# Kernel tuning notes

Measured on AMD Instinct MI355X. Metric: run time of the kernel, lower is better.

The kernel has to match this reference:

```python
import jax, jax.numpy as jnp
import numpy as np

N_NODES = 50000
N_EDGES = 600000
N_PAIRS = 200000
D_IN, D_HID = 128, 256


def _sage_conv(x, src, dst, W_l, b_l, W_r, num_nodes):
    # PyG SAGEConv('mean'): out = mean_agg(x_j) @ W_l + b_l + x @ W_r
    msgs = x[src]                                              # [E, d] gather
    agg = jax.ops.segment_sum(msgs, dst, num_segments=num_nodes)
    deg = jax.ops.segment_sum(jnp.ones((src.shape[0],), x.dtype), dst,
                              num_segments=num_nodes)
    agg = agg / jnp.maximum(deg, 1.0)[:, None]                 # mean, safe for deg=0
    return agg @ W_l + b_l + x @ W_r


def setup_inputs() -> dict:
    key = jax.random.key(0)
    ks = jax.random.split(key, 8)
    s = lambda d: 1.0 / np.sqrt(d)
    return {
        "features": jax.random.normal(ks[0], (N_NODES, D_IN), jnp.float32),
        "edge_index": jax.random.randint(ks[1], (2, N_EDGES), 0, N_NODES, jnp.int64),
        "mask": jax.random.randint(ks[2], (N_PAIRS, 2), 0, N_NODES, jnp.int64),
        "W1l": jax.random.normal(ks[3], (D_IN, D_HID), jnp.float32) * s(D_IN),
        "b1l": jnp.zeros((D_HID,), jnp.float32),
        "W1r": jax.random.normal(ks[4], (D_IN, D_HID), jnp.float32) * s(D_IN),
        "W2l": jax.random.normal(ks[5], (D_HID, D_IN), jnp.float32) * s(D_HID),
        "b2l": jnp.zeros((D_IN,), jnp.float32),
        "W2r": jax.random.normal(ks[6], (D_HID, D_IN), jnp.float32) * s(D_HID),
        "Wlin": jax.random.normal(ks[7], (2 * D_IN, 1), jnp.float32) * s(2 * D_IN),
        "blin": jnp.zeros((1,), jnp.float32),
    }


def reference(features, edge_index, mask, W1l, b1l, W1r, W2l, b2l, W2r, Wlin, blin):
    n = features.shape[0]
    src, dst = edge_index[0], edge_index[1]
    h = _sage_conv(features, src, dst, W1l, b1l, W1r, n)       # [N, 256]
    h = jax.nn.relu(h)                                         # dropout p=0 -> identity
    h = _sage_conv(h, src, dst, W2l, b2l, W2r, n)              # [N, 128]
    m = mask.T                                                 # [2, P]
    p1 = jax.lax.stop_gradient(h[m[0]])                        # detach in original
    p2 = jax.lax.stop_gradient(h[m[1]])
    pair = jnp.concatenate((p1, p2), axis=1)                   # [P, 256]
    return jax.nn.sigmoid(pair @ Wlin + blin)                  # [P, 1]
```

## Files before the change

### kernel.cpp

```cpp
#include <hip/hip_runtime.h>
#include <math.h>

#define NN 50000
#define NE 600000
#define NP 200000
#define NB_SCAN 49

typedef unsigned int uint;
typedef unsigned short ushort;
typedef __attribute__((ext_vector_type(8))) short bf16x8;
typedef __attribute__((ext_vector_type(4))) float f32x4;

__device__ __forceinline__ ushort f2bf(float f) {
    uint u = __float_as_uint(f);
    uint r = (u + 0x7FFFu + ((u >> 16) & 1u)) >> 16;
    return (ushort)r;
}
__device__ __forceinline__ float bf2f(uint lo16) {
    return __uint_as_float(lo16 << 16);
}

__device__ __forceinline__ int wave_iscan(int v, int lane) {
#pragma unroll
    for (int off = 1; off < 64; off <<= 1) {
        int t = __shfl_up(v, off, 64);
        if (lane >= off) v += t;
    }
    return v;
}

typedef const __attribute__((address_space(1))) uint* gas_ptr;
typedef __attribute__((address_space(3))) uint* las_ptr;
__device__ __forceinline__ void gload_lds16(const uint* g, uint* l) {
    __builtin_amdgcn_global_load_lds((gas_ptr)(void*)g, (las_ptr)(void*)l, 16, 0, 0);
}

__device__ __forceinline__ void acc8(float* a, uint4 v) {
    a[0] += bf2f(v.x & 0xffffu); a[1] += bf2f(v.x >> 16);
    a[2] += bf2f(v.y & 0xffffu); a[3] += bf2f(v.y >> 16);
    a[4] += bf2f(v.z & 0xffffu); a[5] += bf2f(v.z >> 16);
    a[6] += bf2f(v.w & 0xffffu); a[7] += bf2f(v.w >> 16);
}

template <int K, int N>
__device__ __forceinline__ void prepB_one(int idx, const float* __restrict__ Wt,
                                          const float* __restrict__ Wb,
                                          ushort* __restrict__ Bp) {
    int lane = idx & 63;
    int nt = (idx >> 6) % (N / 16);
    int ct = idx / (64 * (N / 16));
    int n = nt * 16 + (lane & 15);
    int kb = ct * 32 + (lane >> 4) * 8;
#pragma unroll
    for (int j = 0; j < 8; j++) {
        int k = kb + j;
        float w = (k < K / 2) ? Wt[(size_t)k * N + n] : Wb[(size_t)(k - K / 2) * N + n];
        Bp[(size_t)idx * 8 + j] = f2bf(w);
    }
}

#define T_PREP (NN * 32)
#define T_DEG  (T_PREP + NE)
#define T_B1   (T_DEG + 8192)
#define T_PQ   (T_B1 + 1024)
#define T_CAB  (T_PQ + 2)
__global__ void k_pre(const float* __restrict__ x, uint* __restrict__ xb,
                      const int* __restrict__ dst, int* __restrict__ deg,
                      const float* __restrict__ W1l, const float* __restrict__ W1r,
                      ushort* __restrict__ Bp1,
                      const float* __restrict__ W2l, const float* __restrict__ W2r,
                      const float* __restrict__ Wlin, const float* __restrict__ b2l,
                      float* __restrict__ pq, float* __restrict__ cab) {
    int t = blockIdx.x * 256 + threadIdx.x;
    if (t < T_PREP) {
        int n = t >> 5, c4 = t & 31;
        float4 v = *(const float4*)(x + (size_t)n * 128 + c4 * 4);
        uint2 o;
        o.x = (uint)f2bf(v.x) | ((uint)f2bf(v.y) << 16);
        o.y = (uint)f2bf(v.z) | ((uint)f2bf(v.w) << 16);
        *(uint2*)(xb + (size_t)n * 64 + c4 * 2) = o;
    } else if (t < T_DEG) {
        atomicAdd(deg + dst[t - T_PREP], 1);
    } else if (t < T_B1) {
        prepB_one<256, 256>(t - T_DEG, W1l, W1r, Bp1);
    } else if (t < T_PQ) {
        int idx = t - T_B1;
        int vec = idx >> 8;
        int k = idx & 255;
        const float* W = (vec < 2) ? W2l : W2r;
        const float* wl = Wlin + (vec & 1) * 128;
        float s = 0.f;
#pragma unroll 4
        for (int j = 0; j < 128; j++) s += W[(size_t)k * 128 + j] * wl[j];
        pq[idx] = s;
    } else if (t < T_CAB) {
        int i = t - T_PQ;
        float s = 0.f;
        for (int j = 0; j < 128; j++) s += b2l[j] * Wlin[i * 128 + j];
        cab[i] = s;
    }
}

__global__ __launch_bounds__(1024) void k_scan(const int* __restrict__ deg,
                                               int* __restrict__ bsum,
                                               int* __restrict__ flags,
                                               int* __restrict__ rowptr,
                                               int* __restrict__ cursor) {
    int tid = threadIdx.x;
    int i = blockIdx.x * 1024 + tid;
    int lane = tid & 63, wid = tid >> 6;
    int v = (i < NN) ? deg[i] : 0;
    int incl = wave_iscan(v, lane);
    __shared__ int wt[16];
    __shared__ int sboff;
    if (lane == 63) wt[wid] = incl;
    __syncthreads();
    if (tid < 16) {
        int w = wt[tid];
#pragma unroll
        for (int off = 1; off < 16; off <<= 1) {
            int t = __shfl_up(w, off, 64);
            if (tid >= off) w += t;
        }
        wt[tid] = w;
    }
    __syncthreads();
    int base = (wid > 0) ? wt[wid - 1] : 0;
    int excl_local = incl - v + base;
    if (tid == 0)
        __hip_atomic_store(&bsum[blockIdx.x], wt[15], __ATOMIC_RELEASE,
                           __HIP_MEMORY_SCOPE_AGENT);
    __syncthreads();
    if (tid == 0) {
        __hip_atomic_fetch_add(&flags[0], 1, __ATOMIC_ACQ_REL, __HIP_MEMORY_SCOPE_AGENT);
        while (__hip_atomic_load(&flags[0], __ATOMIC_ACQUIRE,
                                 __HIP_MEMORY_SCOPE_AGENT) < NB_SCAN) {}
    }
    __syncthreads();
    if (tid < 64) {
        int b = (tid < NB_SCAN && tid < (int)blockIdx.x)
                    ? __hip_atomic_load(&bsum[tid], __ATOMIC_ACQUIRE,
                                        __HIP_MEMORY_SCOPE_AGENT)
                    : 0;
#pragma unroll
        for (int off = 1; off < 64; off <<= 1) b += __shfl_xor(b, off, 64);
        if (tid == 0) sboff = b;
    }
    __syncthreads();
    int boff = sboff;
    if (i < NN) {
        int rv = excl_local + boff;
        rowptr[i] = rv;
        cursor[i] = rv;
    }
    if (i == 0) rowptr[NN] = NE;
}

__global__ void k_fill(const int* __restrict__ src, const int* __restrict__ dst,
                       int* __restrict__ cursor, int* __restrict__ ssrc) {
    int e0 = (blockIdx.x * 256 + threadIdx.x) * 4;
    if (e0 >= NE) return;
    int4 d4 = *(const int4*)(dst + e0);
    int4 s4 = *(const int4*)(src + e0);
    int p0 = atomicAdd(cursor + d4.x, 1);
    int p1 = atomicAdd(cursor + d4.y, 1);
    int p2 = atomicAdd(cursor + d4.z, 1);
    int p3 = atomicAdd(cursor + d4.w, 1);
    ssrc[p0] = s4.x;
    ssrc[p1] = s4.y;
    ssrc[p2] = s4.z;
    ssrc[p3] = s4.w;
}

__global__ void k_agg1(const uint* __restrict__ xb, uint* __restrict__ aggb,
                       const int* __restrict__ rowptr, const int* __restrict__ ssrc) {
    int t = blockIdx.x * 256 + threadIdx.x;
    int n = t >> 6;
    if (n >= NN) return;
    int lane = t & 63;
    int g = lane >> 4;
    int s = lane & 15;
    int r0 = rowptr[n], r1 = rowptr[n + 1];
    float a0[8] = {0.f, 0.f, 0.f, 0.f, 0.f, 0.f, 0.f, 0.f};
    float a1[8] = {0.f, 0.f, 0.f, 0.f, 0.f, 0.f, 0.f, 0.f};
    int e = r0;
    for (; e + 16 <= r1; e += 16) {
        int i0 = ssrc[e + g];
        int i1 = ssrc[e + 4 + g];
        int i2 = ssrc[e + 8 + g];
        int i3 = ssrc[e + 12 + g];
        uint4 v0 = *(const uint4*)(xb + (size_t)i0 * 64 + s * 4);
        uint4 v1 = *(const uint4*)(xb + (size_t)i1 * 64 + s * 4);
        uint4 v2 = *(const uint4*)(xb + (size_t)i2 * 64 + s * 4);
        uint4 v3 = *(const uint4*)(xb + (size_t)i3 * 64 + s * 4);
        acc8(a0, v0); acc8(a1, v1); acc8(a0, v2); acc8(a1, v3);
    }
    if (e + 8 <= r1) {
        int i0 = ssrc[e + g];
        int i1 = ssrc[e + 4 + g];
        uint4 v0 = *(const uint4*)(xb + (size_t)i0 * 64 + s * 4);
        uint4 v1 = *(const uint4*)(xb + (size_t)i1 * 64 + s * 4);
        acc8(a0, v0); acc8(a1, v1);
        e += 8;
    }
    if (e + 4 <= r1) {
        int i0 = ssrc[e + g];
        uint4 v0 = *(const uint4*)(xb + (size_t)i0 * 64 + s * 4);
        acc8(a0, v0);
        e += 4;
    }
    int rem = r1 - e;
    if (g < rem) {
        int i0 = ssrc[e + g];
        uint4 v0 = *(const uint4*)(xb + (size_t)i0 * 64 + s * 4);
        acc8(a1, v0);
    }
    float ax[8];
#pragma unroll
    for (int j = 0; j < 8; j++) ax[j] = a0[j] + a1[j];
#pragma unroll
    for (int j = 0; j < 8; j++) {
        ax[j] += __shfl_xor(ax[j], 16, 64);
        ax[j] += __shfl_xor(ax[j], 32, 64);
    }
    if (g == 0) {
        float sc = 1.0f / fmaxf((float)(r1 - r0), 1.0f);
        uint4 o;
        o.x = (uint)f2bf(ax[0] * sc) | ((uint)f2bf(ax[1] * sc) << 16);
        o.y = (uint)f2bf(ax[2] * sc) | ((uint)f2bf(ax[3] * sc) << 16);
        o.z = (uint)f2bf(ax[4] * sc) | ((uint)f2bf(ax[5] * sc) << 16);
        o.w = (uint)f2bf(ax[6] * sc) | ((uint)f2bf(ax[7] * sc) << 16);
        *(uint4*)(aggb + (size_t)n * 64 + s * 4) = o;
    }
}

__global__ __launch_bounds__(256) void k_gemm1(const uint* __restrict__ agg,
                                               const uint* __restrict__ xbu,
                                               const ushort* __restrict__ Bp,
                                               const float* __restrict__ bias,
                                               const float* __restrict__ pq,
                                               float2* __restrict__ g2,
                                               float2* __restrict__ u2) {
    __shared__ uint Af[16 * 256];
    __shared__ float red[4][4][32];
    const int NTW = 4;
    int wave = threadIdx.x >> 6;
    int lane = threadIdx.x & 63;
    int quad = lane >> 4;
    int l15 = lane & 15;
    int mbase = blockIdx.x * 32;

#pragma unroll
    for (int i = 0; i < 4; i++) {
        int chunk = wave * 4 + i;
        int rt = chunk >> 3;
        int ct = chunk & 7;
        int node = mbase + rt * 16 + l15;
        if (node >= NN) node = NN - 1;
        const uint* srcp = ((ct < 4) ? agg : xbu)
                           + (size_t)node * 64 + (ct & 3) * 16 + quad * 4;
        gload_lds16(srcp, &Af[chunk * 256 + lane * 4]);
    }
    __syncthreads();

    f32x4 acc0[NTW], acc1[NTW];
#pragma unroll
    for (int i = 0; i < NTW; i++) {
        acc0[i] = (f32x4){0.f, 0.f, 0.f, 0.f};
        acc1[i] = (f32x4){0.f, 0.f, 0.f, 0.f};
    }
    const bf16x8* bp = (const bf16x8*)Bp;
#pragma unroll
    for (int ct = 0; ct < 8; ct++) {
        bf16x8 a0 = *(const bf16x8*)(&Af[ct * 256 + lane * 4]);
        bf16x8 a1 = *(const bf16x8*)(&Af[(8 + ct) * 256 + lane * 4]);
#pragma unroll
        for (int ntl = 0; ntl < NTW; ntl++) {
            int nt = wave * NTW + ntl;
            bf16x8 b = bp[(ct * 16 + nt) * 64 + lane];
            acc0[ntl] = __builtin_amdgcn_mfma_f32_16x16x32_bf16(a0, b, acc0[ntl], 0, 0, 0);
            acc1[ntl] = __builtin_amdgcn_mfma_f32_16x16x32_bf16(a1, b, acc1[ntl], 0, 0, 0);
        }
    }
    float pga[2][4] = {{0,0,0,0},{0,0,0,0}}, pgb[2][4] = {{0,0,0,0},{0,0,0,0}};
    float pua[2][4] = {{0,0,0,0},{0,0,0,0}}, pub[2][4] = {{0,0,0,0},{0,0,0,0}};
#pragma unroll
    for (int ntl = 0; ntl < NTW; ntl++) {
        int col = (wave * NTW + ntl) * 16 + l15;
        float bv = bias[col];
        float wpa = pq[col], wpb = pq[256 + col];
        float wqa = pq[512 + col], wqb = pq[768 + col];
#pragma unroll
        for (int reg = 0; reg < 4; reg++) {
            float v0 = acc0[ntl][reg] + bv;  v0 = v0 > 0.f ? v0 : 0.f;
            float v1 = acc1[ntl][reg] + bv;  v1 = v1 > 0.f ? v1 : 0.f;
            pga[0][reg] += v0 * wpa;  pgb[0][reg] += v0 * wpb;
            pua[0][reg] += v0 * wqa;  pub[0][reg] += v0 * wqb;
            pga[1][reg] += v1 * wpa;  pgb[1][reg] += v1 * wpb;
            pua[1][reg] += v1 * wqa;  pub[1][reg] += v1 * wqb;
        }
    }
#pragma unroll
    for (int off = 1; off < 16; off <<= 1) {
#pragma unroll
        for (int rt = 0; rt < 2; rt++) {
#pragma unroll
            for (int reg = 0; reg < 4; reg++) {
                pga[rt][reg] += __shfl_xor(pga[rt][reg], off, 64);
                pgb[rt][reg] += __shfl_xor(pgb[rt][reg], off, 64);
                pua[rt][reg] += __shfl_xor(pua[rt][reg], off, 64);
                pub[rt][reg] += __shfl_xor(pub[rt][reg], off, 64);
            }
        }
    }
    if (l15 == 0) {
#pragma unroll
        for (int rt = 0; rt < 2; rt++) {
#pragma unroll
            for (int reg = 0; reg < 4; reg++) {
                int row = rt * 16 + quad * 4 + reg;
                red[0][wave][row] = pga[rt][reg];
                red[1][wave][row] = pgb[rt][reg];
                red[2][wave][row] = pua[rt][reg];
                red[3][wave][row] = pub[rt][reg];
            }
        }
    }
    __syncthreads();
    if (threadIdx.x < 32) {
        int row = threadIdx.x;
        int m = mbase + row;
        if (m < NN) {
            float ga = (red[0][0][row] + red[0][1][row]) + (red[0][2][row] + red[0][3][row]);
            float gb = (red[1][0][row] + red[1][1][row]) + (red[1][2][row] + red[1][3][row]);
            float ua = (red[2][0][row] + red[2][1][row]) + (red[2][2][row] + red[2][3][row]);
            float ub = (red[3][0][row] + red[3][1][row]) + (red[3][2][row] + red[3][3][row]);
            g2[m] = make_float2(ga, gb);
            u2[m] = make_float2(ua, ub);
        }
    }
}

__global__ void k_sagg(const float2* __restrict__ g2, const float2* __restrict__ u2,
                       const int* __restrict__ rowptr, const int* __restrict__ ssrc,
                       const float* __restrict__ cab,
                       float* __restrict__ sa, float* __restrict__ sb) {
    int n = blockIdx.x * 256 + threadIdx.x;
    if (n >= NN) return;
    int r0 = rowptr[n], r1 = rowptr[n + 1];
    float a0 = 0.f, b0 = 0.f, a1 = 0.f, b1 = 0.f;
    float a2 = 0.f, b2 = 0.f, a3 = 0.f, b3 = 0.f;
    int e = r0;
    for (; e + 4 <= r1; e += 4) {
        float2 v0 = g2[ssrc[e]];
        float2 v1 = g2[ssrc[e + 1]];
        float2 v2 = g2[ssrc[e + 2]];
        float2 v3 = g2[ssrc[e + 3]];
        a0 += v0.x; b0 += v0.y;
        a1 += v1.x; b1 += v1.y;
        a2 += v2.x; b2 += v2.y;
        a3 += v3.x; b3 += v3.y;
    }
    for (; e < r1; e++) {
        float2 v = g2[ssrc[e]];
        a0 += v.x; b0 += v.y;
    }
    float sc = 1.0f / fmaxf((float)(r1 - r0), 1.0f);
    float2 u = u2[n];
    sa[n] = ((a0 + a1) + (a2 + a3)) * sc + u.x + cab[0];
    sb[n] = ((b0 + b1) + (b2 + b3)) * sc + u.y + cab[1];
}

__global__ void k_pairs(const float* __restrict__ sa, const float* __restrict__ sb,
                        const int* __restrict__ mask, const float* __restrict__ blin,
                        float* __restrict__ out) {
    int p = blockIdx.x * 256 + threadIdx.x;
    if (p >= NP) return;
    int2 m = ((const int2*)mask)[p];
    float v = sa[m.x] + sb[m.y] + blin[0];
    out[p] = 1.0f / (1.0f + __expf(-v));
}

extern "C" void kernel_launch(void* const* d_in, const int* in_sizes, int n_in,
                              void* d_out, int out_size, void* d_ws, size_t ws_size,
                              hipStream_t stream) {
    const float* x    = (const float*)d_in[0];
    const int*   ei   = (const int*)  d_in[1];
    const int*   mask = (const int*)  d_in[2];
    const float* W1l  = (const float*)d_in[3];
    const float* b1l  = (const float*)d_in[4];
    const float* W1r  = (const float*)d_in[5];
    const float* W2l  = (const float*)d_in[6];
    const float* b2l  = (const float*)d_in[7];
    const float* W2r  = (const float*)d_in[8];
    const float* Wlin = (const float*)d_in[9];
    const float* blin = (const float*)d_in[10];
    float* out = (float*)d_out;

    const int* src = ei;
    const int* dst = ei + NE;

    char* ws = (char*)d_ws;
    int*    deg    = (int*)(ws);
    int*    flags  = (int*)(ws + 0xF0000);
    int*    rowptr = (int*)(ws + (size_t)1 * (1 << 20));
    int*    cursor = (int*)(ws + (size_t)2 * (1 << 20));
    int*    ssrc   = (int*)(ws + (size_t)3 * (1 << 20));
    int*    bsum   = (int*)(ws + (size_t)6 * (1 << 20));
    ushort* Bp1    = (ushort*)(ws + (size_t)8 * (1 << 20));
    float*  pq     = (float*)(ws + (size_t)9 * (1 << 20));
    float*  cab    = (float*)(ws + (size_t)9 * (1 << 20) + 65536);
    float*  sa     = (float*)(ws + (size_t)10 * (1 << 20));
    float*  sb     = (float*)(ws + (size_t)11 * (1 << 20));
    float2* g2     = (float2*)(ws + (size_t)12 * (1 << 20));
    float2* u2     = (float2*)(ws + (size_t)13 * (1 << 20));
    uint*   xb     = (uint*)(ws + (size_t)14 * (1 << 20));
    uint*   aggb   = (uint*)(ws + (size_t)28 * (1 << 20));

    hipMemsetAsync(ws, 0, (size_t)1 << 20, stream);

    k_pre  <<<(T_CAB + 255) / 256, 256, 0, stream>>>(x, xb, dst, deg,
                                                     W1l, W1r, Bp1,
                                                     W2l, W2r, Wlin, b2l, pq, cab);
    k_scan <<<NB_SCAN, 1024, 0, stream>>>(deg, bsum, flags, rowptr, cursor);
    k_fill <<<(NE / 4 + 255) / 256, 256, 0, stream>>>(src, dst, cursor, ssrc);
    k_agg1 <<<NN / 4, 256, 0, stream>>>(xb, aggb, rowptr, ssrc);
    k_gemm1<<<(NN + 31) / 32, 256, 0, stream>>>(aggb, xb, Bp1, b1l, pq, g2, u2);
    k_sagg <<<(NN + 255) / 256, 256, 0, stream>>>(g2, u2, rowptr, ssrc, cab, sa, sb);
    k_pairs<<<(NP + 255) / 256, 256, 0, stream>>>(sa, sb, mask, blin, out);
}
```

Baseline: 216.6 us.

## Partition CSR fill by destination range and double rows per GEMM block

The CSR fill kernel now splits edges into chunks and launches 8 partitions per chunk. Each block reads its chunk of edges but only scatters edges whose destination falls in its node range, which keeps atomic and scatter traffic local to a smaller region of memory (intended for L2 locality). The cost is reading src/dst 8 times. Separately, the first-layer GEMM processes 64 rows per block instead of 32, so each B-fragment load feeds twice as many MFMAs, at the cost of more registers and LDS and fewer blocks.

```diff
diff --git a/kernel.cpp b/kernel.cpp
--- a/kernel.cpp
+++ b/kernel.cpp
@@ -5,6 +5,10 @@
 #define NE 600000
 #define NP 200000
 #define NB_SCAN 49
+#define NPART 8
+#define PART_N (NN / NPART)
+#define FILL_CHUNKS 75
+#define CHUNK_E (NE / FILL_CHUNKS)
 
 typedef unsigned int uint;
 typedef unsigned short ushort;
@@ -158,18 +162,19 @@
 
 __global__ void k_fill(const int* __restrict__ src, const int* __restrict__ dst,
                        int* __restrict__ cursor, int* __restrict__ ssrc) {
-    int e0 = (blockIdx.x * 256 + threadIdx.x) * 4;
-    if (e0 >= NE) return;
-    int4 d4 = *(const int4*)(dst + e0);
-    int4 s4 = *(const int4*)(src + e0);
-    int p0 = atomicAdd(cursor + d4.x, 1);
-    int p1 = atomicAdd(cursor + d4.y, 1);
-    int p2 = atomicAdd(cursor + d4.z, 1);
-    int p3 = atomicAdd(cursor + d4.w, 1);
-    ssrc[p0] = s4.x;
-    ssrc[p1] = s4.y;
-    ssrc[p2] = s4.z;
-    ssrc[p3] = s4.w;
+    int part = blockIdx.x & 7;
+    int chunk = blockIdx.x >> 3;
+    int lo = part * PART_N;
+    int e_begin = chunk * CHUNK_E;
+    int e_end = e_begin + CHUNK_E;
+    for (int e0 = e_begin + threadIdx.x * 4; e0 < e_end; e0 += 1024) {
+        int4 d4 = *(const int4*)(dst + e0);
+        int4 s4 = *(const int4*)(src + e0);
+        if ((uint)(d4.x - lo) < (uint)PART_N) ssrc[atomicAdd(cursor + d4.x, 1)] = s4.x;
+        if ((uint)(d4.y - lo) < (uint)PART_N) ssrc[atomicAdd(cursor + d4.y, 1)] = s4.y;
+        if ((uint)(d4.z - lo) < (uint)PART_N) ssrc[atomicAdd(cursor + d4.z, 1)] = s4.z;
+        if ((uint)(d4.w - lo) < (uint)PART_N) ssrc[atomicAdd(cursor + d4.w, 1)] = s4.w;
+    }
 }
 
 __global__ void k_agg1(const uint* __restrict__ xb, uint* __restrict__ aggb,
@@ -241,18 +246,18 @@
                                                const float* __restrict__ pq,
                                                float2* __restrict__ g2,
                                                float2* __restrict__ u2) {
-    __shared__ uint Af[16 * 256];
-    __shared__ float red[4][4][32];
+    __shared__ uint Af[32 * 256];
+    __shared__ float red[4][4][64];
     const int NTW = 4;
     int wave = threadIdx.x >> 6;
     int lane = threadIdx.x & 63;
     int quad = lane >> 4;
     int l15 = lane & 15;
-    int mbase = blockIdx.x * 32;
-
-#pragma unroll
-    for (int i = 0; i < 4; i++) {
-        int chunk = wave * 4 + i;
+    int mbase = blockIdx.x * 64;
+
+#pragma unroll
+    for (int i = 0; i < 8; i++) {
+        int chunk = wave * 8 + i;
         int rt = chunk >> 3;
         int ct = chunk & 7;
         int node = mbase + rt * 16 + l15;
@@ -263,27 +268,36 @@
     }
     __syncthreads();
 
-    f32x4 acc0[NTW], acc1[NTW];
-#pragma unroll
-    for (int i = 0; i < NTW; i++) {
-        acc0[i] = (f32x4){0.f, 0.f, 0.f, 0.f};
-        acc1[i] = (f32x4){0.f, 0.f, 0.f, 0.f};
-    }
+    f32x4 acc[4][NTW];
+#pragma unroll
+    for (int rt = 0; rt < 4; rt++)
+#pragma unroll
+        for (int i = 0; i < NTW; i++) acc[rt][i] = (f32x4){0.f, 0.f, 0.f, 0.f};
     const bf16x8* bp = (const bf16x8*)Bp;
 #pragma unroll
     for (int ct = 0; ct < 8; ct++) {
-        bf16x8 a0 = *(const bf16x8*)(&Af[ct * 256 + lane * 4]);
-        bf16x8 a1 = *(const bf16x8*)(&Af[(8 + ct) * 256 + lane * 4]);
+        bf16x8 a0 = *(const bf16x8*)(&Af[(0 * 8 + ct) * 256 + lane * 4]);
+        bf16x8 a1 = *(const bf16x8*)(&Af[(1 * 8 + ct) * 256 + lane * 4]);
+        bf16x8 a2 = *(const bf16x8*)(&Af[(2 * 8 + ct) * 256 + lane * 4]);
+        bf16x8 a3 = *(const bf16x8*)(&Af[(3 * 8 + ct) * 256 + lane * 4]);
 #pragma unroll
         for (int ntl = 0; ntl < NTW; ntl++) {
             int nt = wave * NTW + ntl;
             bf16x8 b = bp[(ct * 16 + nt) * 64 + lane];
-            acc0[ntl] = __builtin_amdgcn_mfma_f32_16x16x32_bf16(a0, b, acc0[ntl], 0, 0, 0);
-            acc1[ntl] = __builtin_amdgcn_mfma_f32_16x16x32_bf16(a1, b, acc1[ntl], 0, 0, 0);
-        }
-    }
-    float pga[2][4] = {{0,0,0,0},{0,0,0,0}}, pgb[2][4] = {{0,0,0,0},{0,0,0,0}};
-    float pua[2][4] = {{0,0,0,0},{0,0,0,0}}, pub[2][4] = {{0,0,0,0},{0,0,0,0}};
+            acc[0][ntl] = __builtin_amdgcn_mfma_f32_16x16x32_bf16(a0, b, acc[0][ntl], 0, 0, 0);
+            acc[1][ntl] = __builtin_amdgcn_mfma_f32_16x16x32_bf16(a1, b, acc[1][ntl], 0, 0, 0);
+            acc[2][ntl] = __builtin_amdgcn_mfma_f32_16x16x32_bf16(a2, b, acc[2][ntl], 0, 0, 0);
+            acc[3][ntl] = __builtin_amdgcn_mfma_f32_16x16x32_bf16(a3, b, acc[3][ntl], 0, 0, 0);
+        }
+    }
+    float pga[4][4], pgb[4][4], pua[4][4], pub[4][4];
+#pragma unroll
+    for (int rt = 0; rt < 4; rt++)
+#pragma unroll
+        for (int reg = 0; reg < 4; reg++) {
+            pga[rt][reg] = 0.f; pgb[rt][reg] = 0.f;
+            pua[rt][reg] = 0.f; pub[rt][reg] = 0.f;
+        }
 #pragma unroll
     for (int ntl = 0; ntl < NTW; ntl++) {
         int col = (wave * NTW + ntl) * 16 + l15;
@@ -291,19 +305,20 @@
         float wpa = pq[col], wpb = pq[256 + col];
         float wqa = pq[512 + col], wqb = pq[768 + col];
 #pragma unroll
-        for (int reg = 0; reg < 4; reg++) {
-            float v0 = acc0[ntl][reg] + bv;  v0 = v0 > 0.f ? v0 : 0.f;
-            float v1 = acc1[ntl][reg] + bv;  v1 = v1 > 0.f ? v1 : 0.f;
-            pga[0][reg] += v0 * wpa;  pgb[0][reg] += v0 * wpb;
-            pua[0][reg] += v0 * wqa;  pub[0][reg] += v0 * wqb;
-            pga[1][reg] += v1 * wpa;  pgb[1][reg] += v1 * wpb;
-            pua[1][reg] += v1 * wqa;  pub[1][reg] += v1 * wqb;
+        for (int rt = 0; rt < 4; rt++) {
+#pragma unroll
+            for (int reg = 0; reg < 4; reg++) {
+                float v = acc[rt][ntl][reg] + bv;
+                v = v > 0.f ? v : 0.f;
+                pga[rt][reg] += v * wpa;  pgb[rt][reg] += v * wpb;
+                pua[rt][reg] += v * wqa;  pub[rt][reg] += v * wqb;
+            }
         }
     }
 #pragma unroll
     for (int off = 1; off < 16; off <<= 1) {
 #pragma unroll
-        for (int rt = 0; rt < 2; rt++) {
+        for (int rt = 0; rt < 4; rt++) {
 #pragma unroll
             for (int reg = 0; reg < 4; reg++) {
                 pga[rt][reg] += __shfl_xor(pga[rt][reg], off, 64);
@@ -315,7 +330,7 @@
     }
     if (l15 == 0) {
 #pragma unroll
-        for (int rt = 0; rt < 2; rt++) {
+        for (int rt = 0; rt < 4; rt++) {
 #pragma unroll
             for (int reg = 0; reg < 4; reg++) {
                 int row = rt * 16 + quad * 4 + reg;
@@ -327,7 +342,7 @@
         }
     }
     __syncthreads();
-    if (threadIdx.x < 32) {
+    if (threadIdx.x < 64) {
         int row = threadIdx.x;
         int m = mbase + row;
         if (m < NN) {
@@ -423,9 +438,9 @@
                                                      W1l, W1r, Bp1,
                                                      W2l, W2r, Wlin, b2l, pq, cab);
     k_scan <<<NB_SCAN, 1024, 0, stream>>>(deg, bsum, flags, rowptr, cursor);
-    k_fill <<<(NE / 4 + 255) / 256, 256, 0, stream>>>(src, dst, cursor, ssrc);
+    k_fill <<<FILL_CHUNKS * NPART, 256, 0, stream>>>(src, dst, cursor, ssrc);
     k_agg1 <<<NN / 4, 256, 0, stream>>>(xb, aggb, rowptr, ssrc);
-    k_gemm1<<<(NN + 31) / 32, 256, 0, stream>>>(aggb, xb, Bp1, b1l, pq, g2, u2);
+    k_gemm1<<<(NN + 63) / 64, 256, 0, stream>>>(aggb, xb, Bp1, b1l, pq, g2, u2);
     k_sagg <<<(NN + 255) / 256, 256, 0, stream>>>(g2, u2, rowptr, ssrc, cab, sa, sb);
     k_pairs<<<(NP + 255) / 256, 256, 0, stream>>>(sa, sb, mask, blin, out);
 }
```

New measurement: 220.5 us. No clear change (+1.8%).
